# Performance work log

Measured on AMD Instinct MI355X. Metric: run time of the kernel, lower is better.

Reference implementation:

```python
import jax, jax.numpy as jnp
import numpy as np

N = 50000      # nodes
E = 800000     # edges (before self-loops)
H = 4          # attention heads
C = 32         # out_features per head
DIN = 128      # in_features (== H*C so residual path is active)
ED = 16        # edge_dim
NEG = 0.2      # LeakyReLU negative slope (GATConv default)
EPS = 1e-5     # LayerNorm eps


def setup_inputs() -> dict:
    key = jax.random.key(0)
    ks = jax.random.split(key, 12)
    s = 0.05
    return {
        "x": jax.random.normal(ks[0], (N, DIN), dtype=jnp.float32),
        "edge_index": jax.random.randint(ks[1], (2, E), 0, N, dtype=jnp.int64),
        "edge_attr": jax.random.normal(ks[2], (E, ED), dtype=jnp.float32),
        # edge_processor: Linear(ED, ED) + ReLU (dropout = identity at eval)
        "W_ep": jax.random.normal(ks[3], (ED, ED), dtype=jnp.float32) * s,
        "b_ep": jnp.zeros((ED,), dtype=jnp.float32),
        # GATConv params (lin / lin_edge are bias-free in PyG)
        "W_lin": jax.random.normal(ks[4], (DIN, H * C), dtype=jnp.float32) * s,
        "W_edge": jax.random.normal(ks[5], (ED, H * C), dtype=jnp.float32) * s,
        "att_src": jax.random.normal(ks[6], (H, C), dtype=jnp.float32) * s,
        "att_dst": jax.random.normal(ks[7], (H, C), dtype=jnp.float32) * s,
        "att_edge": jax.random.normal(ks[8], (H, C), dtype=jnp.float32) * s,
        "bias": jnp.zeros((H * C,), dtype=jnp.float32),
        # LayerNorm params
        "ln_g": jnp.ones((H * C,), dtype=jnp.float32),
        "ln_b": jnp.zeros((H * C,), dtype=jnp.float32),
    }


def reference(x, edge_index, edge_attr, W_ep, b_ep, W_lin, W_edge,
              att_src, att_dst, att_edge, bias, ln_g, ln_b):
    n = x.shape[0]
    src, dst = edge_index[0], edge_index[1]

    # edge_processor: Linear + ReLU
    ea = jax.nn.relu(edge_attr @ W_ep + b_ep)                       # [E, ED]

    # add self-loops (PyG GATConv default), loop edge_attr = mean of incoming
    ones = jnp.ones((ea.shape[0],), dtype=ea.dtype)
    deg = jax.ops.segment_sum(ones, dst, num_segments=n)            # [N]
    loop_attr = jax.ops.segment_sum(ea, dst, num_segments=n)
    loop_attr = loop_attr / jnp.maximum(deg, 1.0)[:, None]          # [N, ED]
    loop = jnp.arange(n, dtype=src.dtype)
    src2 = jnp.concatenate([src, loop])                             # [E+N]
    dst2 = jnp.concatenate([dst, loop])
    ea2 = jnp.concatenate([ea, loop_attr], axis=0)                  # [E+N, ED]

    # node / edge linear transforms
    h = (x @ W_lin).reshape(n, H, C)                                # [N, H, C]
    a_src = jnp.einsum('nhc,hc->nh', h, att_src)                    # [N, H]
    a_dst = jnp.einsum('nhc,hc->nh', h, att_dst)
    e = (ea2 @ W_edge).reshape(-1, H, C)                            # [E+N, H, C]
    a_e = jnp.einsum('ehc,hc->eh', e, att_edge)                     # [E+N, H]

    # per-edge attention logits + leaky relu
    alpha = a_src[src2] + a_dst[dst2] + a_e                         # [E+N, H]
    alpha = jnp.where(alpha >= 0, alpha, NEG * alpha)

    # segment softmax over incoming edges of each dst node
    m = jax.ops.segment_max(alpha, dst2, num_segments=n)            # [N, H]
    ex = jnp.exp(alpha - m[dst2])
    denom = jax.ops.segment_sum(ex, dst2, num_segments=n)           # [N, H]
    w = ex / denom[dst2]                                            # [E+N, H]

    # scatter-aggregate messages
    msg = h[src2] * w[:, :, None]                                   # [E+N, H, C]
    out = jax.ops.segment_sum(msg, dst2, num_segments=n)            # [N, H, C]
    out = out.reshape(n, H * C) + bias

    # residual (DIN == H*C) + LayerNorm
    out = out + x
    mu = jnp.mean(out, axis=-1, keepdims=True)
    var = jnp.var(out, axis=-1, keepdims=True)
    out = (out - mu) * jax.lax.rsqrt(var + EPS) * ln_g + ln_b
    return out
```

## Files before the change

kernel.cpp:

```cpp
#include <hip/hip_runtime.h>
#include <hip/hip_fp16.h>
#include <math.h>

#define NN   50000
#define EE   800000
#define HH   4
#define CC   32
#define DINN 128
#define ED   16
#define NEGS 0.2f
#define LNEPS 1e-5f
#define SCAN_NB ((NN + 255) / 256)

struct __align__(16) Hp4 { __half2 a, b, c, d; };

__global__ __launch_bounds__(256, 3) void k_node(
        const float* __restrict__ x, const float* __restrict__ W_lin,
        const float* __restrict__ att_src, const float* __restrict__ att_dst,
        __half* __restrict__ hb, float* __restrict__ a_src, float* __restrict__ a_dst) {
    __shared__ float xr[64 * 132];
    int t = threadIdx.x;
    int row0 = blockIdx.x * 64;

    #pragma unroll
    for (int i = 0; i < 8; ++i) {
        int idx = t + 256 * i;
        int r = idx >> 5, kq = idx & 31;
        int row = row0 + r;
        float4 v = make_float4(0.f, 0.f, 0.f, 0.f);
        if (row < NN) v = ((const float4*)x)[(long)row * 32 + kq];
        *(float4*)&xr[r * 132 + kq * 4] = v;
    }
    __syncthreads();

    int colg = t & 15, rowg = t >> 4;
    int c0 = colg * 8;
    const float* Wp = W_lin + c0;
    float acc[4][8] = {};

    #pragma unroll 2
    for (int k = 0; k < DINN; k += 2) {
        float4 wa0 = *(const float4*)&Wp[(long)k * DINN];
        float4 wb0 = *(const float4*)&Wp[(long)k * DINN + 4];
        float4 wa1 = *(const float4*)&Wp[(long)(k + 1) * DINN];
        float4 wb1 = *(const float4*)&Wp[(long)(k + 1) * DINN + 4];
        #pragma unroll
        for (int i = 0; i < 4; ++i) {
            float2 xv = *(const float2*)&xr[(rowg * 4 + i) * 132 + k];
            acc[i][0] = fmaf(xv.x, wa0.x, acc[i][0]);
            acc[i][1] = fmaf(xv.x, wa0.y, acc[i][1]);
            acc[i][2] = fmaf(xv.x, wa0.z, acc[i][2]);
            acc[i][3] = fmaf(xv.x, wa0.w, acc[i][3]);
            acc[i][4] = fmaf(xv.x, wb0.x, acc[i][4]);
            acc[i][5] = fmaf(xv.x, wb0.y, acc[i][5]);
            acc[i][6] = fmaf(xv.x, wb0.z, acc[i][6]);
            acc[i][7] = fmaf(xv.x, wb0.w, acc[i][7]);
            acc[i][0] = fmaf(xv.y, wa1.x, acc[i][0]);
            acc[i][1] = fmaf(xv.y, wa1.y, acc[i][1]);
            acc[i][2] = fmaf(xv.y, wa1.z, acc[i][2]);
            acc[i][3] = fmaf(xv.y, wa1.w, acc[i][3]);
            acc[i][4] = fmaf(xv.y, wb1.x, acc[i][4]);
            acc[i][5] = fmaf(xv.y, wb1.y, acc[i][5]);
            acc[i][6] = fmaf(xv.y, wb1.z, acc[i][6]);
            acc[i][7] = fmaf(xv.y, wb1.w, acc[i][7]);
        }
    }

    int head = colg >> 2;
    int cw = c0 & 31;
    float4 as0 = *(const float4*)&att_src[head * CC + cw];
    float4 as1 = *(const float4*)&att_src[head * CC + cw + 4];
    float4 ad0 = *(const float4*)&att_dst[head * CC + cw];
    float4 ad1 = *(const float4*)&att_dst[head * CC + cw + 4];
    #pragma unroll
    for (int i = 0; i < 4; ++i) {
        int row = row0 + rowg * 4 + i;
        if (row < NN) {
            Hp4 p;
            p.a = __floats2half2_rn(acc[i][0], acc[i][1]);
            p.b = __floats2half2_rn(acc[i][2], acc[i][3]);
            p.c = __floats2half2_rn(acc[i][4], acc[i][5]);
            p.d = __floats2half2_rn(acc[i][6], acc[i][7]);
            *(Hp4*)&hb[(long)row * DINN + c0] = p;
        }
        float ps = acc[i][0]*as0.x + acc[i][1]*as0.y + acc[i][2]*as0.z + acc[i][3]*as0.w
                 + acc[i][4]*as1.x + acc[i][5]*as1.y + acc[i][6]*as1.z + acc[i][7]*as1.w;
        float pd = acc[i][0]*ad0.x + acc[i][1]*ad0.y + acc[i][2]*ad0.z + acc[i][3]*ad0.w
                 + acc[i][4]*ad1.x + acc[i][5]*ad1.y + acc[i][6]*ad1.z + acc[i][7]*ad1.w;
        ps += __shfl_xor(ps, 1); ps += __shfl_xor(ps, 2);
        pd += __shfl_xor(pd, 1); pd += __shfl_xor(pd, 2);
        if ((colg & 3) == 0 && row < NN) {
            a_src[row * 4 + head] = ps;
            a_dst[row * 4 + head] = pd;
        }
    }
}

__global__ __launch_bounds__(256) void k_edgeA(
        const int* __restrict__ ei, const float* __restrict__ edge_attr,
        const float* __restrict__ W_ep, const float* __restrict__ b_ep,
        const float* __restrict__ W_edge, const float* __restrict__ att_edge,
        const float* __restrict__ a_src, const float* __restrict__ a_dst,
        int* __restrict__ cnt, int* __restrict__ rank,
        uint4* __restrict__ payload) {
    __shared__ float Wl[ED * ED];
    __shared__ float bl[ED];
    __shared__ float vl[ED * 4];
    int t = threadIdx.x;
    if (t < ED * ED) Wl[t] = W_ep[t];
    if (t < ED) bl[t] = b_ep[t];
    if (t >= 192 && t < 192 + 64) {
        int q = t - 192;
        int d = q >> 2, h = q & 3;
        float s = 0.f;
        #pragma unroll 8
        for (int c = 0; c < CC; ++c)
            s += W_edge[d * (HH * CC) + h * CC + c] * att_edge[h * CC + c];
        vl[q] = s;
    }
    __syncthreads();

    int e = blockIdx.x * 256 + t;
    if (e >= EE) return;

    int src = ei[e];
    int dst = ei[EE + e];

    float a[ED];
    const float4* ap = (const float4*)(edge_attr + (long)e * ED);
    float4 a0 = ap[0], a1 = ap[1], a2 = ap[2], a3 = ap[3];
    a[0]=a0.x; a[1]=a0.y; a[2]=a0.z; a[3]=a0.w;
    a[4]=a1.x; a[5]=a1.y; a[6]=a1.z; a[7]=a1.w;
    a[8]=a2.x; a[9]=a2.y; a[10]=a2.z; a[11]=a2.w;
    a[12]=a3.x; a[13]=a3.y; a[14]=a3.z; a[15]=a3.w;

    float4 s4 = *(const float4*)&a_src[src * 4];
    float4 d4 = *(const float4*)&a_dst[dst * 4];

    float r[ED];
    #pragma unroll
    for (int j = 0; j < ED; ++j) r[j] = bl[j];
    #pragma unroll
    for (int d = 0; d < ED; ++d) {
        float av = a[d];
        #pragma unroll
        for (int j = 0; j < ED; ++j) r[j] = fmaf(av, Wl[d * ED + j], r[j]);
    }

    float ae0 = 0.f, ae1 = 0.f, ae2 = 0.f, ae3 = 0.f;
    #pragma unroll
    for (int d = 0; d < ED; ++d) {
        float rd = fmaxf(r[d], 0.f);
        ae0 = fmaf(rd, vl[d * 4 + 0], ae0);
        ae1 = fmaf(rd, vl[d * 4 + 1], ae1);
        ae2 = fmaf(rd, vl[d * 4 + 2], ae2);
        ae3 = fmaf(rd, vl[d * 4 + 3], ae3);
    }

    float v0 = s4.x + d4.x + ae0;
    float v1 = s4.y + d4.y + ae1;
    float v2 = s4.z + d4.z + ae2;
    float v3 = s4.w + d4.w + ae3;
    v0 = (v0 >= 0.f) ? v0 : NEGS * v0;
    v1 = (v1 >= 0.f) ? v1 : NEGS * v1;
    v2 = (v2 >= 0.f) ? v2 : NEGS * v2;
    v3 = (v3 >= 0.f) ? v3 : NEGS * v3;

    __half2 p0 = __floats2half2_rn(__expf(v0), ae0);
    __half2 p1 = __floats2half2_rn(__expf(v1), ae1);
    __half2 p2 = __floats2half2_rn(__expf(v2), ae2);
    __half2 p3 = __floats2half2_rn(__expf(v3), ae3);
    payload[e] = make_uint4(*(unsigned*)&p0, *(unsigned*)&p1,
                            *(unsigned*)&p2, *(unsigned*)&p3);
    rank[e] = atomicAdd(cnt + dst, 1);
}

__global__ __launch_bounds__(256) void k_scanA(const int* __restrict__ cnt,
                                               int* __restrict__ partial) {
    int t = threadIdx.x, b = blockIdx.x;
    int i = b * 256 + t;
    int v = (i < NN) ? cnt[i] : 0;
    #pragma unroll
    for (int d = 1; d < 64; d <<= 1) v += __shfl_xor(v, d);
    __shared__ int wt[4];
    if ((t & 63) == 0) wt[t >> 6] = v;
    __syncthreads();
    if (t == 0) partial[b] = wt[0] + wt[1] + wt[2] + wt[3];
}

__global__ __launch_bounds__(256) void k_scanB(const int* __restrict__ partial,
                                               int* __restrict__ poff,
                                               int* __restrict__ row_start) {
    int t = threadIdx.x;
    int lane = t & 63, w = t >> 6;
    int v = (t < SCAN_NB) ? partial[t] : 0;
    int sv = v;
    #pragma unroll
    for (int d = 1; d < 64; d <<= 1) {
        int o = __shfl_up(sv, d);
        if (lane >= d) sv += o;
    }
    __shared__ int wt[4];
    if (lane == 63) wt[w] = sv;
    __syncthreads();
    int base = 0;
    for (int j = 0; j < w; ++j) base += wt[j];
    if (t < SCAN_NB) poff[t] = base + sv - v;
    if (t == 255) row_start[NN] = wt[0] + wt[1] + wt[2] + wt[3];
}

__global__ __launch_bounds__(256) void k_scanC(const int* __restrict__ cnt,
                                               const int* __restrict__ poff,
                                               int* __restrict__ row_start) {
    int t = threadIdx.x, b = blockIdx.x;
    int i = b * 256 + t;
    int v = (i < NN) ? cnt[i] : 0;
    int lane = t & 63, w = t >> 6;
    int sv = v;
    #pragma unroll
    for (int d = 1; d < 64; d <<= 1) {
        int o = __shfl_up(sv, d);
        if (lane >= d) sv += o;
    }
    __shared__ int wt[4];
    if (lane == 63) wt[w] = sv;
    __syncthreads();
    int base = 0;
    for (int j = 0; j < w; ++j) base += wt[j];
    if (i < NN) row_start[i] = poff[b] + base + sv - v;
}

__global__ __launch_bounds__(256) void k_edgeB(
        const int* __restrict__ ei, const uint4* __restrict__ payload,
        const int* __restrict__ rank, const int* __restrict__ row_start,
        uint4* __restrict__ pk, int* __restrict__ csr_src) {
    int base = (blockIdx.x * 256 + threadIdx.x) * 4;
    if (base + 3 < EE) {
        int4 s4 = *(const int4*)(ei + base);
        int4 d4 = *(const int4*)(ei + EE + base);
        int4 r4 = *(const int4*)(rank + base);
        uint4 p0 = payload[base], p1 = payload[base + 1];
        uint4 p2 = payload[base + 2], p3 = payload[base + 3];
        int q0 = row_start[d4.x] + r4.x;
        int q1 = row_start[d4.y] + r4.y;
        int q2 = row_start[d4.z] + r4.z;
        int q3 = row_start[d4.w] + r4.w;
        pk[q0] = p0; pk[q1] = p1; pk[q2] = p2; pk[q3] = p3;
        csr_src[q0] = s4.x; csr_src[q1] = s4.y;
        csr_src[q2] = s4.z; csr_src[q3] = s4.w;
    } else {
        for (int e = base; e < EE; ++e) {
            int q = row_start[ei[EE + e]] + rank[e];
            pk[q] = payload[e];
            csr_src[q] = ei[e];
        }
    }
}

__global__ __launch_bounds__(256) void k_aggregate(
        const float* __restrict__ x, const __half2* __restrict__ hb,
        const float* __restrict__ a_src, const float* __restrict__ a_dst,
        const int* __restrict__ row_start,
        const unsigned* __restrict__ pkh, const int* __restrict__ srcs,
        const float* __restrict__ bias, const float* __restrict__ ln_g,
        const float* __restrict__ ln_b, float* __restrict__ out) {
    int t = threadIdx.x;
    int wave = t >> 6, lane = t & 63;
    int n = blockIdx.x * 4 + wave;
    if (n >= NN) return;

    int start = row_start[n];
    int deg   = row_start[n + 1] - start;
    int head  = lane >> 4;

    float accx = 0.f, accy = 0.f, s_own = 0.f, aes_own = 0.f;
    const unsigned* pp = pkh + (size_t)start * 4 + head;
    const int* sp = srcs + start;

    int k = 0;
    for (; k + 8 <= deg; k += 8) {
        unsigned pv[8]; int sv[8];
        #pragma unroll
        for (int j = 0; j < 8; ++j) {
            pv[j] = pp[(size_t)(k + j) * 4];
            sv[j] = sp[k + j];
        }
        __half2 hv[8];
        #pragma unroll
        for (int j = 0; j < 8; ++j) hv[j] = hb[(long)sv[j] * 64 + lane];
        #pragma unroll
        for (int j = 0; j < 8; ++j) {
            float2 wf = __half22float2(*(__half2*)&pv[j]);
            s_own += wf.x;
            aes_own += wf.y;
            float2 hf = __half22float2(hv[j]);
            accx = fmaf(wf.x, hf.x, accx);
            accy = fmaf(wf.x, hf.y, accy);
        }
    }
    for (; k < deg; ++k) {
        unsigned p = pp[(size_t)k * 4];
        int src = sp[k];
        __half2 hv = hb[(long)src * 64 + lane];
        float2 wf = __half22float2(*(__half2*)&p);
        s_own += wf.x;
        aes_own += wf.y;
        float2 hf = __half22float2(hv);
        accx = fmaf(wf.x, hf.x, accx);
        accy = fmaf(wf.x, hf.y, accy);
    }

    float inv_deg = 1.0f / fmaxf((float)deg, 1.0f);
    float v = a_src[n * 4 + head] + a_dst[n * 4 + head] + aes_own * inv_deg;
    v = (v >= 0.f) ? v : NEGS * v;
    float w0 = __expf(v);
    s_own += w0;
    float2 hn = __half22float2(hb[(long)n * 64 + lane]);
    accx = fmaf(w0, hn.x, accx);
    accy = fmaf(w0, hn.y, accy);
    float is = 1.0f / s_own;
    accx *= is; accy *= is;

    int c0 = lane * 2;
    float2 b2 = *(const float2*)&bias[c0];
    float2 x2 = *(const float2*)&x[(long)n * DINN + c0];
    float oa = accx + b2.x + x2.x;
    float ob = accy + b2.y + x2.y;
    float sum = oa + ob, sumsq = oa * oa + ob * ob;
    #pragma unroll
    for (int d2 = 1; d2 < 64; d2 <<= 1) {
        sum   += __shfl_xor(sum, d2);
        sumsq += __shfl_xor(sumsq, d2);
    }
    float mu  = sum * (1.0f / DINN);
    float var = sumsq * (1.0f / DINN) - mu * mu;
    float rs  = rsqrtf(var + LNEPS);
    float2 g2  = *(const float2*)&ln_g[c0];
    float2 lb2 = *(const float2*)&ln_b[c0];
    float2 o2;
    o2.x = (oa - mu) * rs * g2.x + lb2.x;
    o2.y = (ob - mu) * rs * g2.y + lb2.y;
    *(float2*)&out[(long)n * DINN + c0] = o2;
}

extern "C" void kernel_launch(void* const* d_in, const int* in_sizes, int n_in,
                              void* d_out, int out_size, void* d_ws, size_t ws_size,
                              hipStream_t stream) {
    const float* x         = (const float*)d_in[0];
    const int*   ei        = (const int*)d_in[1];
    const float* edge_attr = (const float*)d_in[2];
    const float* W_ep      = (const float*)d_in[3];
    const float* b_ep      = (const float*)d_in[4];
    const float* W_lin     = (const float*)d_in[5];
    const float* W_edge    = (const float*)d_in[6];
    const float* att_src   = (const float*)d_in[7];
    const float* att_dst   = (const float*)d_in[8];
    const float* att_edge  = (const float*)d_in[9];
    const float* bias      = (const float*)d_in[10];
    const float* ln_g      = (const float*)d_in[11];
    const float* ln_b      = (const float*)d_in[12];
    float* out = (float*)d_out;

    char* ws = (char*)d_ws;
    size_t o = 0;
    auto take = [&](size_t bytes) -> char* {
        char* p = ws + o;
        o = (o + bytes + 255) & ~(size_t)255;
        return p;
    };
    __half* hbuf      = (__half*)take((size_t)NN * DINN * 2);
    float*  a_src     = (float*)take((size_t)NN * 4 * 4);
    float*  a_dst     = (float*)take((size_t)NN * 4 * 4);
    int*    cnt       = (int*)  take((size_t)NN * 4);
    int*    row_start = (int*)  take((size_t)(NN + 1) * 4);
    int*    rank      = (int*)  take((size_t)EE * 4);
    int*    partial   = (int*)  take((size_t)SCAN_NB * 4);
    int*    poff      = (int*)  take((size_t)SCAN_NB * 4);
    uint4*  payload   = (uint4*)take((size_t)EE * 16);
    uint4*  pk        = (uint4*)take((size_t)EE * 16);
    int*    csr_src   = (int*)  take((size_t)EE * 4);

    hipMemsetAsync(cnt, 0, (size_t)NN * 4, stream);

    k_node<<<(NN + 63) / 64, 256, 0, stream>>>(x, W_lin, att_src, att_dst,
                                               hbuf, a_src, a_dst);
    k_edgeA<<<(EE + 255) / 256, 256, 0, stream>>>(ei, edge_attr, W_ep, b_ep,
                                                  W_edge, att_edge, a_src, a_dst,
                                                  cnt, rank, payload);
    k_scanA<<<SCAN_NB, 256, 0, stream>>>(cnt, partial);
    k_scanB<<<1, 256, 0, stream>>>(partial, poff, row_start);
    k_scanC<<<SCAN_NB, 256, 0, stream>>>(cnt, poff, row_start);
    k_edgeB<<<(EE / 4 + 255) / 256, 256, 0, stream>>>(ei, payload, rank,
                                                      row_start, pk, csr_src);
    k_aggregate<<<(NN + 3) / 4, 256, 0, stream>>>(x, (const __half2*)hbuf,
                                                  a_src, a_dst, row_start,
                                                  (const unsigned*)pk, csr_src,
                                                  bias, ln_g, ln_b, out);
}
```

Before: 284.5 us.

## Scatter edge ids instead of payloads, pad atomic counters, process two edges per thread

```diff
diff --git a/kernel.cpp b/kernel.cpp
--- a/kernel.cpp
+++ b/kernel.cpp
@@ -11,6 +11,7 @@
 #define NEGS 0.2f
 #define LNEPS 1e-5f
 #define SCAN_NB ((NN + 255) / 256)
+#define CPAD 32
 
 struct __align__(16) Hp4 { __half2 a, b, c, d; };
 
@@ -120,66 +121,73 @@
     }
     __syncthreads();
 
-    int e = blockIdx.x * 256 + t;
-    if (e >= EE) return;
-
-    int src = ei[e];
-    int dst = ei[EE + e];
-
-    float a[ED];
-    const float4* ap = (const float4*)(edge_attr + (long)e * ED);
-    float4 a0 = ap[0], a1 = ap[1], a2 = ap[2], a3 = ap[3];
-    a[0]=a0.x; a[1]=a0.y; a[2]=a0.z; a[3]=a0.w;
-    a[4]=a1.x; a[5]=a1.y; a[6]=a1.z; a[7]=a1.w;
-    a[8]=a2.x; a[9]=a2.y; a[10]=a2.z; a[11]=a2.w;
-    a[12]=a3.x; a[13]=a3.y; a[14]=a3.z; a[15]=a3.w;
-
-    float4 s4 = *(const float4*)&a_src[src * 4];
-    float4 d4 = *(const float4*)&a_dst[dst * 4];
-
-    float r[ED];
-    #pragma unroll
-    for (int j = 0; j < ED; ++j) r[j] = bl[j];
-    #pragma unroll
-    for (int d = 0; d < ED; ++d) {
-        float av = a[d];
-        #pragma unroll
-        for (int j = 0; j < ED; ++j) r[j] = fmaf(av, Wl[d * ED + j], r[j]);
-    }
-
-    float ae0 = 0.f, ae1 = 0.f, ae2 = 0.f, ae3 = 0.f;
-    #pragma unroll
-    for (int d = 0; d < ED; ++d) {
-        float rd = fmaxf(r[d], 0.f);
-        ae0 = fmaf(rd, vl[d * 4 + 0], ae0);
-        ae1 = fmaf(rd, vl[d * 4 + 1], ae1);
-        ae2 = fmaf(rd, vl[d * 4 + 2], ae2);
-        ae3 = fmaf(rd, vl[d * 4 + 3], ae3);
-    }
-
-    float v0 = s4.x + d4.x + ae0;
-    float v1 = s4.y + d4.y + ae1;
-    float v2 = s4.z + d4.z + ae2;
-    float v3 = s4.w + d4.w + ae3;
-    v0 = (v0 >= 0.f) ? v0 : NEGS * v0;
-    v1 = (v1 >= 0.f) ? v1 : NEGS * v1;
-    v2 = (v2 >= 0.f) ? v2 : NEGS * v2;
-    v3 = (v3 >= 0.f) ? v3 : NEGS * v3;
-
-    __half2 p0 = __floats2half2_rn(__expf(v0), ae0);
-    __half2 p1 = __floats2half2_rn(__expf(v1), ae1);
-    __half2 p2 = __floats2half2_rn(__expf(v2), ae2);
-    __half2 p3 = __floats2half2_rn(__expf(v3), ae3);
-    payload[e] = make_uint4(*(unsigned*)&p0, *(unsigned*)&p1,
-                            *(unsigned*)&p2, *(unsigned*)&p3);
-    rank[e] = atomicAdd(cnt + dst, 1);
+    int e0 = blockIdx.x * 512 + t;
+
+    #pragma unroll
+    for (int u = 0; u < 2; ++u) {
+        int e = e0 + u * 256;
+        if (e >= EE) break;
+
+        int src = ei[e];
+        int dst = ei[EE + e];
+
+        float a[ED];
+        const float4* ap = (const float4*)(edge_attr + (long)e * ED);
+        float4 a0 = ap[0], a1 = ap[1], a2 = ap[2], a3 = ap[3];
+        a[0]=a0.x; a[1]=a0.y; a[2]=a0.z; a[3]=a0.w;
+        a[4]=a1.x; a[5]=a1.y; a[6]=a1.z; a[7]=a1.w;
+        a[8]=a2.x; a[9]=a2.y; a[10]=a2.z; a[11]=a2.w;
+        a[12]=a3.x; a[13]=a3.y; a[14]=a3.z; a[15]=a3.w;
+
+        float4 s4 = *(const float4*)&a_src[src * 4];
+        float4 d4 = *(const float4*)&a_dst[dst * 4];
+
+        int rk = atomicAdd(cnt + (long)dst * CPAD, 1);
+
+        float r[ED];
+        #pragma unroll
+        for (int j = 0; j < ED; ++j) r[j] = bl[j];
+        #pragma unroll
+        for (int d = 0; d < ED; ++d) {
+            float av = a[d];
+            #pragma unroll
+            for (int j = 0; j < ED; ++j) r[j] = fmaf(av, Wl[d * ED + j], r[j]);
+        }
+
+        float ae0 = 0.f, ae1 = 0.f, ae2 = 0.f, ae3 = 0.f;
+        #pragma unroll
+        for (int d = 0; d < ED; ++d) {
+            float rd = fmaxf(r[d], 0.f);
+            ae0 = fmaf(rd, vl[d * 4 + 0], ae0);
+            ae1 = fmaf(rd, vl[d * 4 + 1], ae1);
+            ae2 = fmaf(rd, vl[d * 4 + 2], ae2);
+            ae3 = fmaf(rd, vl[d * 4 + 3], ae3);
+        }
+
+        float v0 = s4.x + d4.x + ae0;
+        float v1 = s4.y + d4.y + ae1;
+        float v2 = s4.z + d4.z + ae2;
+        float v3 = s4.w + d4.w + ae3;
+        v0 = (v0 >= 0.f) ? v0 : NEGS * v0;
+        v1 = (v1 >= 0.f) ? v1 : NEGS * v1;
+        v2 = (v2 >= 0.f) ? v2 : NEGS * v2;
+        v3 = (v3 >= 0.f) ? v3 : NEGS * v3;
+
+        __half2 p0 = __floats2half2_rn(__expf(v0), ae0);
+        __half2 p1 = __floats2half2_rn(__expf(v1), ae1);
+        __half2 p2 = __floats2half2_rn(__expf(v2), ae2);
+        __half2 p3 = __floats2half2_rn(__expf(v3), ae3);
+        payload[e] = make_uint4(*(unsigned*)&p0, *(unsigned*)&p1,
+                                *(unsigned*)&p2, *(unsigned*)&p3);
+        rank[e] = rk;
+    }
 }
 
 __global__ __launch_bounds__(256) void k_scanA(const int* __restrict__ cnt,
                                                int* __restrict__ partial) {
     int t = threadIdx.x, b = blockIdx.x;
     int i = b * 256 + t;
-    int v = (i < NN) ? cnt[i] : 0;
+    int v = (i < NN) ? cnt[(long)i * CPAD] : 0;
     #pragma unroll
     for (int d = 1; d < 64; d <<= 1) v += __shfl_xor(v, d);
     __shared__ int wt[4];
@@ -214,7 +222,7 @@
                                                int* __restrict__ row_start) {
     int t = threadIdx.x, b = blockIdx.x;
     int i = b * 256 + t;
-    int v = (i < NN) ? cnt[i] : 0;
+    int v = (i < NN) ? cnt[(long)i * CPAD] : 0;
     int lane = t & 63, w = t >> 6;
     int sv = v;
     #pragma unroll
@@ -231,37 +239,27 @@
 }
 
 __global__ __launch_bounds__(256) void k_edgeB(
-        const int* __restrict__ ei, const uint4* __restrict__ payload,
-        const int* __restrict__ rank, const int* __restrict__ row_start,
-        uint4* __restrict__ pk, int* __restrict__ csr_src) {
+        const int* __restrict__ ei, const int* __restrict__ rank,
+        const int* __restrict__ row_start, int* __restrict__ csr_eid) {
     int base = (blockIdx.x * 256 + threadIdx.x) * 4;
     if (base + 3 < EE) {
-        int4 s4 = *(const int4*)(ei + base);
         int4 d4 = *(const int4*)(ei + EE + base);
         int4 r4 = *(const int4*)(rank + base);
-        uint4 p0 = payload[base], p1 = payload[base + 1];
-        uint4 p2 = payload[base + 2], p3 = payload[base + 3];
-        int q0 = row_start[d4.x] + r4.x;
-        int q1 = row_start[d4.y] + r4.y;
-        int q2 = row_start[d4.z] + r4.z;
-        int q3 = row_start[d4.w] + r4.w;
-        pk[q0] = p0; pk[q1] = p1; pk[q2] = p2; pk[q3] = p3;
-        csr_src[q0] = s4.x; csr_src[q1] = s4.y;
-        csr_src[q2] = s4.z; csr_src[q3] = s4.w;
+        csr_eid[row_start[d4.x] + r4.x] = base;
+        csr_eid[row_start[d4.y] + r4.y] = base + 1;
+        csr_eid[row_start[d4.z] + r4.z] = base + 2;
+        csr_eid[row_start[d4.w] + r4.w] = base + 3;
     } else {
-        for (int e = base; e < EE; ++e) {
-            int q = row_start[ei[EE + e]] + rank[e];
-            pk[q] = payload[e];
-            csr_src[q] = ei[e];
-        }
+        for (int e = base; e < EE; ++e)
+            csr_eid[row_start[ei[EE + e]] + rank[e]] = e;
     }
 }
 
 __global__ __launch_bounds__(256) void k_aggregate(
         const float* __restrict__ x, const __half2* __restrict__ hb,
         const float* __restrict__ a_src, const float* __restrict__ a_dst,
-        const int* __restrict__ row_start,
-        const unsigned* __restrict__ pkh, const int* __restrict__ srcs,
+        const int* __restrict__ row_start, const int* __restrict__ csr_eid,
+        const unsigned* __restrict__ pkh, const int* __restrict__ ei,
         const float* __restrict__ bias, const float* __restrict__ ln_g,
         const float* __restrict__ ln_b, float* __restrict__ out) {
     int t = threadIdx.x;
@@ -274,16 +272,18 @@
     int head  = lane >> 4;
 
     float accx = 0.f, accy = 0.f, s_own = 0.f, aes_own = 0.f;
-    const unsigned* pp = pkh + (size_t)start * 4 + head;
-    const int* sp = srcs + start;
+    const int* ep = csr_eid + start;
 
     int k = 0;
     for (; k + 8 <= deg; k += 8) {
+        int ev[8];
+        #pragma unroll
+        for (int j = 0; j < 8; ++j) ev[j] = ep[k + j];
         unsigned pv[8]; int sv[8];
         #pragma unroll
         for (int j = 0; j < 8; ++j) {
-            pv[j] = pp[(size_t)(k + j) * 4];
-            sv[j] = sp[k + j];
+            pv[j] = pkh[(size_t)ev[j] * 4 + head];
+            sv[j] = ei[ev[j]];
         }
         __half2 hv[8];
         #pragma unroll
@@ -299,8 +299,9 @@
         }
     }
     for (; k < deg; ++k) {
-        unsigned p = pp[(size_t)k * 4];
-        int src = sp[k];
+        int e = ep[k];
+        unsigned p = pkh[(size_t)e * 4 + head];
+        int src = ei[e];
         __half2 hv = hb[(long)src * 64 + lane];
         float2 wf = __half22float2(*(__half2*)&p);
         s_own += wf.x;
@@ -371,29 +372,27 @@
     __half* hbuf      = (__half*)take((size_t)NN * DINN * 2);
     float*  a_src     = (float*)take((size_t)NN * 4 * 4);
     float*  a_dst     = (float*)take((size_t)NN * 4 * 4);
-    int*    cnt       = (int*)  take((size_t)NN * 4);
+    int*    cnt       = (int*)  take((size_t)NN * CPAD * 4);
     int*    row_start = (int*)  take((size_t)(NN + 1) * 4);
     int*    rank      = (int*)  take((size_t)EE * 4);
     int*    partial   = (int*)  take((size_t)SCAN_NB * 4);
     int*    poff      = (int*)  take((size_t)SCAN_NB * 4);
     uint4*  payload   = (uint4*)take((size_t)EE * 16);
-    uint4*  pk        = (uint4*)take((size_t)EE * 16);
-    int*    csr_src   = (int*)  take((size_t)EE * 4);
-
-    hipMemsetAsync(cnt, 0, (size_t)NN * 4, stream);
+    int*    csr_eid   = (int*)  take((size_t)EE * 4);
+
+    hipMemsetAsync(cnt, 0, (size_t)NN * CPAD * 4, stream);
 
     k_node<<<(NN + 63) / 64, 256, 0, stream>>>(x, W_lin, att_src, att_dst,
                                                hbuf, a_src, a_dst);
-    k_edgeA<<<(EE + 255) / 256, 256, 0, stream>>>(ei, edge_attr, W_ep, b_ep,
+    k_edgeA<<<(EE + 511) / 512, 256, 0, stream>>>(ei, edge_attr, W_ep, b_ep,
                                                   W_edge, att_edge, a_src, a_dst,
                                                   cnt, rank, payload);
     k_scanA<<<SCAN_NB, 256, 0, stream>>>(cnt, partial);
     k_scanB<<<1, 256, 0, stream>>>(partial, poff, row_start);
     k_scanC<<<SCAN_NB, 256, 0, stream>>>(cnt, poff, row_start);
-    k_edgeB<<<(EE / 4 + 255) / 256, 256, 0, stream>>>(ei, payload, rank,
-                                                      row_start, pk, csr_src);
+    k_edgeB<<<(EE / 4 + 255) / 256, 256, 0, stream>>>(ei, rank, row_start, csr_eid);
     k_aggregate<<<(NN + 3) / 4, 256, 0, stream>>>(x, (const __half2*)hbuf,
-                                                  a_src, a_dst, row_start,
-                                                  (const unsigned*)pk, csr_src,
+                                                  a_src, a_dst, row_start, csr_eid,
+                                                  (const unsigned*)payload, ei,
                                                   bias, ln_g, ln_b, out);
 }
```

Result: slower. 293.9 us (+3.3%).
